# Kernel optimization log

Measured on AMD Instinct MI355X. Metric: run time of the kernel, lower is better.

Reference implementation:

```python
import jax, jax.numpy as jnp
import numpy as np

D_MODEL = 1024
N_HEADS = 16
HEAD_DIM = D_MODEL // N_HEADS
Q_PROJ = D_MODEL // 2
KV_PROJ = D_MODEL
INIT_SCALE = 0.02
EPS = 1e-5


def _ln(x, g, b):
    mu = jnp.mean(x, axis=-1, keepdims=True)
    var = jnp.mean(jnp.square(x - mu), axis=-1, keepdims=True)
    return (x - mu) * jax.lax.rsqrt(var + EPS) * g + b


def setup_inputs() -> dict:
    key = jax.random.key(0)
    ks = jax.random.split(key, 8)
    B, S = 2, 2048
    x = jax.random.normal(ks[0], (B, S, D_MODEL), dtype=jnp.float32)
    W_dq = INIT_SCALE * jax.random.normal(ks[1], (D_MODEL, Q_PROJ), dtype=jnp.float32)
    W_uq = INIT_SCALE * jax.random.normal(ks[2], (Q_PROJ, D_MODEL), dtype=jnp.float32)
    W_dkv = INIT_SCALE * jax.random.normal(ks[3], (D_MODEL, KV_PROJ), dtype=jnp.float32)
    W_ukv = INIT_SCALE * jax.random.normal(ks[4], (KV_PROJ, 2 * D_MODEL), dtype=jnp.float32)
    wo = INIT_SCALE * jax.random.normal(ks[5], (D_MODEL, D_MODEL), dtype=jnp.float32)
    return {
        "x": x,
        "W_dq": W_dq, "W_uq": W_uq,
        "q_ln_g": jnp.ones((Q_PROJ,), jnp.float32), "q_ln_b": jnp.zeros((Q_PROJ,), jnp.float32),
        "W_dkv": W_dkv, "W_ukv": W_ukv,
        "kv_ln_g": jnp.ones((KV_PROJ,), jnp.float32), "kv_ln_b": jnp.zeros((KV_PROJ,), jnp.float32),
        "preq_g": jnp.ones((D_MODEL,), jnp.float32), "preq_b": jnp.zeros((D_MODEL,), jnp.float32),
        "prekv_g": jnp.ones((D_MODEL,), jnp.float32), "prekv_b": jnp.zeros((D_MODEL,), jnp.float32),
        "wo": wo,
    }


def reference(x, W_dq, W_uq, q_ln_g, q_ln_b, W_dkv, W_ukv, kv_ln_g, kv_ln_b,
              preq_g, preq_b, prekv_g, prekv_b, wo):
    B, S, D = x.shape
    H, dh = N_HEADS, HEAD_DIM
    # Q path: pre-norm -> low-rank down -> LN -> up
    x_q = _ln(x, preq_g, preq_b)
    cq = _ln(x_q @ W_dq, q_ln_g, q_ln_b)            # [B,S,D/2]
    Q = (cq @ W_uq).reshape(B, S, H, dh)             # [B,S,H,dh]
    Q = Q / jnp.sqrt(jnp.asarray(dh, x.dtype))
    # KV path: pre-norm -> compress -> LN -> up, split into K,V
    x_kv = _ln(x, prekv_g, prekv_b)
    ckv = _ln(x_kv @ W_dkv, kv_ln_g, kv_ln_b)        # [B,S,D]
    KV = ckv @ W_ukv                                 # [B,S,2D]
    K, V = jnp.split(KV, 2, axis=-1)
    K = K.reshape(B, S, H, dh)
    V = V.reshape(B, S, H, dh)
    # causal attention (scores materialized as in original)
    scores = jnp.einsum('bqhd,bkhd->bhqk', Q, K)     # [B,H,S,S]
    causal = jnp.tril(jnp.ones((S, S), dtype=bool))  # True where allowed
    scores = jnp.where(causal[None, None], scores, jnp.asarray(-jnp.inf, scores.dtype))
    attn = jax.nn.softmax(scores, axis=-1)
    out = jnp.einsum('bhqk,bkhd->bqhd', attn, V).reshape(B, S, D)
    return out @ wo.T
```

## Files before the change

kernel.cpp:

```cpp
#include <hip/hip_runtime.h>
#include <hip/hip_bf16.h>

#define SEQ   2048
#define BATCH 2
#define NROWS 4096
#define DM    1024
#define NHEAD 16
#define DH    64
#define QP    512
#define KVP   1024
#define CH    8

typedef unsigned short us;
using bf16x8 = __attribute__((ext_vector_type(8))) __bf16;
using f32x4  = __attribute__((ext_vector_type(4))) float;

__device__ __forceinline__ us f2bf(float f) {
  union { __hip_bfloat16 h; us u; } cv;
  cv.h = __float2bfloat16(f);
  return cv.u;
}
__device__ __forceinline__ float bf2f(us u) {
  union { unsigned int u32; float f; } cv;
  cv.u32 = ((unsigned int)u) << 16;
  return cv.f;
}
__device__ __forceinline__ float loadp(const void* p, long i, int isbf) {
  return isbf ? bf2f(((const us*)p)[i]) : ((const float*)p)[i];
}
__device__ __forceinline__ void async16(const void* g, void* l) {
  __builtin_amdgcn_global_load_lds((__attribute__((address_space(1))) void*)g,
                                   (__attribute__((address_space(3))) void*)l,
                                   16, 0, 0);
}

__global__ void detect_dtype(const us* __restrict__ xu, int* __restrict__ flag) {
  __shared__ int red[256];
  const int tid = threadIdx.x;
  int cnt = 0;
  for (int i = tid; i < 4096; i += 256) {
    const int e = (xu[i] >> 7) & 0xff;
    if (e == 0 || (e >= 100 && e <= 134)) cnt++;
  }
  red[tid] = cnt;
  __syncthreads();
  for (int s = 128; s; s >>= 1) {
    if (tid < s) red[tid] += red[tid + s];
    __syncthreads();
  }
  if (tid == 0) *flag = (red[0] >= 3900) ? 1 : 0;
}

struct TD { const void* in; us* out; int R, C, nt, trans; };

__global__ __launch_bounds__(256) void prep_weights(TD t0, TD t1, TD t2, TD t3, TD t4,
                                                    const int* __restrict__ flag) {
  __shared__ us tile[32][33];
  int lin = blockIdx.x;
  TD t = t0;
  if (lin >= t.nt) { lin -= t.nt; t = t1;
    if (lin >= t.nt) { lin -= t.nt; t = t2;
      if (lin >= t.nt) { lin -= t.nt; t = t3;
        if (lin >= t.nt) { lin -= t.nt; t = t4; } } } }
  const int isbf = *flag;
  const int ntx = t.C >> 5;
  const int by = lin / ntx, bx = lin - by * ntx;
  const int tx = threadIdx.x & 31, ty = threadIdx.x >> 5;
  const long r0 = (long)by * 32, c0 = (long)bx * 32;
  if (t.trans) {
#pragma unroll
    for (int i = 0; i < 32; i += 8)
      tile[ty + i][tx] = isbf ? ((const us*)t.in)[(r0 + ty + i) * t.C + c0 + tx]
                              : f2bf(((const float*)t.in)[(r0 + ty + i) * t.C + c0 + tx]);
    __syncthreads();
#pragma unroll
    for (int i = 0; i < 32; i += 8)
      t.out[(c0 + ty + i) * t.R + r0 + tx] = tile[tx][ty + i];
  } else {
#pragma unroll
    for (int i = 0; i < 32; i += 8)
      t.out[(r0 + ty + i) * t.C + c0 + tx] =
          isbf ? ((const us*)t.in)[(r0 + ty + i) * t.C + c0 + tx]
               : f2bf(((const float*)t.in)[(r0 + ty + i) * t.C + c0 + tx]);
  }
}

__global__ void zero_f32(float4* __restrict__ p, int n4) {
  int i = blockIdx.x * blockDim.x + threadIdx.x;
  const int stride = gridDim.x * blockDim.x;
  const float4 z = {0.f, 0.f, 0.f, 0.f};
  for (; i < n4; i += stride) p[i] = z;
}

__global__ __launch_bounds__(256) void ln_dual(
    const void* __restrict__ xin,
    const void* __restrict__ g1, const void* __restrict__ b1,
    const void* __restrict__ g2, const void* __restrict__ b2,
    us* __restrict__ out1, us* __restrict__ out2,
    const int* __restrict__ flag)
{
  const long row = blockIdx.x;
  const int tid = threadIdx.x;
  const int isbf = *flag;
  float v[4];
  float s = 0.f, s2 = 0.f;
#pragma unroll
  for (int i = 0; i < 4; i++) {
    const long c = tid + i * 256;
    const float t = loadp(xin, row * 1024 + c, isbf);
    v[i] = t; s += t; s2 += t * t;
  }
#pragma unroll
  for (int off = 32; off > 0; off >>= 1) {
    s  += __shfl_down(s,  off);
    s2 += __shfl_down(s2, off);
  }
  __shared__ float red[8];
  __shared__ float musd[2];
  const int wave = tid >> 6, lane = tid & 63;
  if (lane == 0) { red[wave] = s; red[4 + wave] = s2; }
  __syncthreads();
  if (tid == 0) {
    const float ts = red[0] + red[1] + red[2] + red[3];
    const float t2 = red[4] + red[5] + red[6] + red[7];
    const float mu = ts * (1.f / 1024.f);
    const float var = t2 * (1.f / 1024.f) - mu * mu;
    musd[0] = mu; musd[1] = rsqrtf(var + 1e-5f);
  }
  __syncthreads();
  const float mu = musd[0], rs = musd[1];
#pragma unroll
  for (int i = 0; i < 4; i++) {
    const long c = tid + i * 256;
    const float nrm = (v[i] - mu) * rs;
    out1[row * 1024 + c] = f2bf(nrm * loadp(g1, c, isbf) + loadp(b1, c, isbf));
    out2[row * 1024 + c] = f2bf(nrm * loadp(g2, c, isbf) + loadp(b2, c, isbf));
  }
}

template<int C>
__device__ __forceinline__ void ln_body(const us* __restrict__ in,
                                        const void* __restrict__ g, const void* __restrict__ b,
                                        us* __restrict__ out, long row, int tid, int isbf) {
  constexpr int NP = C / 256;
  float v[NP];
  float s = 0.f, s2 = 0.f;
#pragma unroll
  for (int i = 0; i < NP; i++) {
    const float t = bf2f(in[row * C + tid + i * 256]);
    v[i] = t; s += t; s2 += t * t;
  }
#pragma unroll
  for (int off = 32; off > 0; off >>= 1) {
    s  += __shfl_down(s,  off);
    s2 += __shfl_down(s2, off);
  }
  __shared__ float red[8];
  __shared__ float musd[2];
  const int wave = tid >> 6, lane = tid & 63;
  if (lane == 0) { red[wave] = s; red[4 + wave] = s2; }
  __syncthreads();
  if (tid == 0) {
    const float ts = red[0] + red[1] + red[2] + red[3];
    const float t2 = red[4] + red[5] + red[6] + red[7];
    const float mu = ts * (1.f / C);
    const float var = t2 * (1.f / C) - mu * mu;
    musd[0] = mu; musd[1] = rsqrtf(var + 1e-5f);
  }
  __syncthreads();
  const float mu = musd[0], rs = musd[1];
#pragma unroll
  for (int i = 0; i < NP; i++) {
    const long c = tid + i * 256;
    out[row * C + c] = f2bf((v[i] - mu) * rs * loadp(g, c, isbf) + loadp(b, c, isbf));
  }
}

__global__ __launch_bounds__(256) void ln_rows_pair(
    const us* __restrict__ inq, const void* __restrict__ qg, const void* __restrict__ qb,
    us* __restrict__ outq,
    const us* __restrict__ inkv, const void* __restrict__ kvg, const void* __restrict__ kvb,
    us* __restrict__ outkv,
    const int* __restrict__ flag)
{
  const int isbf = *flag;
  if (blockIdx.x < NROWS)
    ln_body<512>(inq, qg, qb, outq, blockIdx.x, threadIdx.x, isbf);
  else
    ln_body<1024>(inkv, kvg, kvb, outkv, blockIdx.x - NROWS, threadIdx.x, isbf);
}

struct GD { const us* A; const us* Bt; void* C; int N, K, nxs; float scale; int omode; };

__global__ __launch_bounds__(256) void gemm_mt(GD g0, GD g1, int nb0,
                                               const int* __restrict__ flag) {
  __shared__ us As[128 * 32];
  __shared__ us Bs[128 * 32];
  GD g;
  int lin = blockIdx.x;
  if (lin < nb0) g = g0; else { g = g1; lin -= nb0; }
  const int by = lin >> g.nxs;
  const int bx = lin - (by << g.nxs);
  const int N = g.N, K = g.K;

  const int tid  = threadIdx.x;
  const int lane = tid & 63;
  const int wave = tid >> 6;
  const int n16  = lane & 15;
  const int quad = lane >> 4;
  const long m0 = (long)by * 128;
  const long n0 = (long)bx * 128;
  const int wm = (wave >> 1) * 64;
  const int wn = (wave & 1) * 64;

  const f32x4 zero = {0.f, 0.f, 0.f, 0.f};
  f32x4 acc[4][4];
#pragma unroll
  for (int i = 0; i < 4; i++)
#pragma unroll
    for (int j = 0; j < 4; j++) acc[i][j] = zero;

  const int srow = tid >> 2;
  const int scol = (tid & 3) * 8;
  const us* Ag0 = g.A  + (m0 + srow) * K + scol;
  const us* Ag1 = g.A  + (m0 + 64 + srow) * K + scol;
  const us* Bg0 = g.Bt + (n0 + srow) * K + scol;
  const us* Bg1 = g.Bt + (n0 + 64 + srow) * K + scol;
  us* As0 = As + srow * 32 + scol;
  us* As1 = As + (64 + srow) * 32 + scol;
  us* Bs0 = Bs + srow * 32 + scol;
  us* Bs1 = Bs + (64 + srow) * 32 + scol;

  for (int k0 = 0; k0 < K; k0 += 32) {
    async16(Ag0 + k0, As0);
    async16(Ag1 + k0, As1);
    async16(Bg0 + k0, Bs0);
    async16(Bg1 + k0, Bs1);
    __syncthreads();
    bf16x8 af[4], bfv[4];
#pragma unroll
    for (int i = 0; i < 4; i++)
      af[i] = *(const bf16x8*)(As + (wm + i * 16 + n16) * 32 + quad * 8);
#pragma unroll
    for (int j = 0; j < 4; j++)
      bfv[j] = *(const bf16x8*)(Bs + (wn + j * 16 + n16) * 32 + quad * 8);
#pragma unroll
    for (int i = 0; i < 4; i++)
#pragma unroll
      for (int j = 0; j < 4; j++)
        acc[i][j] = __builtin_amdgcn_mfma_f32_16x16x32_bf16(af[i], bfv[j], acc[i][j], 0, 0, 0);
    __syncthreads();
  }

  const bool obf = (g.omode == 1) || (g.omode == 2 && *flag != 0);
  float* Cf = (float*)g.C;
  us* Cb = (us*)g.C;
#pragma unroll
  for (int i = 0; i < 4; i++) {
    const long row = m0 + wm + i * 16 + quad * 4;
#pragma unroll
    for (int j = 0; j < 4; j++) {
      const long col = n0 + wn + j * 16 + n16;
#pragma unroll
      for (int r = 0; r < 4; r++) {
        const float v = acc[i][j][r] * g.scale;
        if (obf) Cb[(row + r) * N + col] = f2bf(v);
        else     Cf[(row + r) * N + col] = v;
      }
    }
  }
}

__global__ __launch_bounds__(256) void flash_attn(
    const us* __restrict__ Q, const us* __restrict__ KV,
    float* __restrict__ Oacc, float* __restrict__ Lacc)
{
  __shared__ us Ks[64 * 72];
  __shared__ us Vt[64 * 72];
  __shared__ us Ps[4][16 * 72];

  int lin = blockIdx.x;
  int qt = 31, nc = 0;
  for (; qt >= 0; --qt) { nc = (qt >> 3) + 1; if (lin < nc) break; lin -= nc; }
  const int chunk = lin;
  const int kt0 = chunk * CH;
  const int kt1 = min(kt0 + CH, qt + 1);

  const int h   = blockIdx.y;
  const int bb  = blockIdx.z;
  const int tid = threadIdx.x;
  const int lane = tid & 63;
  const int wave = tid >> 6;
  const int n16 = lane & 15;
  const int quad = lane >> 4;
  const int qbase = qt * 64;
  const long rowQ0 = (long)bb * SEQ;

  bf16x8 aq[2];
  {
    const long gq = (rowQ0 + qbase + wave * 16 + n16) * DM + h * DH;
    aq[0] = *(const bf16x8*)(Q + gq + quad * 8);
    aq[1] = *(const bf16x8*)(Q + gq + 32 + quad * 8);
  }

  const f32x4 zero = {0.f, 0.f, 0.f, 0.f};
  f32x4 oacc[4];
#pragma unroll
  for (int d = 0; d < 4; d++) oacc[d] = zero;
  float rsum[4] = {0.f, 0.f, 0.f, 0.f};

  const int kk_key = tid >> 3;
  const int kk_d8  = (tid & 7) * 8;
  const int vd  = tid & 63;
  const int vkb = (tid >> 6) * 8;

  const us* kgb = KV + (rowQ0 + kk_key) * 2048 + h * DH + kk_d8;
  const us* vgb = KV + (rowQ0 + vkb) * 2048 + KVP + h * DH + vd;

  uint4 kpre0, kpre1;
  us vraw[16];
  auto loadKV = [&](int kt) {
    const us* kg = kgb + (long)kt * (64 * 2048);
    kpre0 = *(const uint4*)kg;
    kpre1 = *(const uint4*)(kg + 32 * 2048);
    const us* vg = vgb + (long)kt * (64 * 2048);
#pragma unroll
    for (int j = 0; j < 8; j++) vraw[j] = vg[j * 2048];
    const us* vg2 = vg + 32 * 2048;
#pragma unroll
    for (int j = 0; j < 8; j++) vraw[8 + j] = vg2[j * 2048];
  };
  loadKV(kt0);

  for (int kt = kt0; kt < kt1; kt++) {
    __syncthreads();
    *(uint4*)(Ks + kk_key * 72 + kk_d8)        = kpre0;
    *(uint4*)(Ks + (kk_key + 32) * 72 + kk_d8) = kpre1;
    {
      uint4 p0, p1;
      p0.x = (unsigned)vraw[0]  | ((unsigned)vraw[1]  << 16);
      p0.y = (unsigned)vraw[2]  | ((unsigned)vraw[3]  << 16);
      p0.z = (unsigned)vraw[4]  | ((unsigned)vraw[5]  << 16);
      p0.w = (unsigned)vraw[6]  | ((unsigned)vraw[7]  << 16);
      p1.x = (unsigned)vraw[8]  | ((unsigned)vraw[9]  << 16);
      p1.y = (unsigned)vraw[10] | ((unsigned)vraw[11] << 16);
      p1.z = (unsigned)vraw[12] | ((unsigned)vraw[13] << 16);
      p1.w = (unsigned)vraw[14] | ((unsigned)vraw[15] << 16);
      *(uint4*)(Vt + vd * 72 + vkb)      = p0;
      *(uint4*)(Vt + vd * 72 + vkb + 32) = p1;
    }
    __syncthreads();
    if (kt + 1 < kt1) loadKV(kt + 1);

    f32x4 sv[4];
#pragma unroll
    for (int j = 0; j < 4; j++) {
      const bf16x8 bk0 = *(const bf16x8*)(Ks + (j * 16 + n16) * 72 + quad * 8);
      const bf16x8 bk1 = *(const bf16x8*)(Ks + (j * 16 + n16) * 72 + 32 + quad * 8);
      f32x4 s = zero;
      s = __builtin_amdgcn_mfma_f32_16x16x32_bf16(aq[0], bk0, s, 0, 0, 0);
      s = __builtin_amdgcn_mfma_f32_16x16x32_bf16(aq[1], bk1, s, 0, 0, 0);
      sv[j] = s;
    }

    const int qrow = qbase + wave * 16 + quad * 4;
    if (kt == qt) {
#pragma unroll
      for (int j = 0; j < 4; j++) {
        const int col = qt * 64 + j * 16 + n16;
#pragma unroll
        for (int r = 0; r < 4; r++)
          sv[j][r] = (col <= qrow + r) ? sv[j][r] : -1e30f;
      }
    }

    us* Pw = Ps[wave];
#pragma unroll
    for (int j = 0; j < 4; j++)
#pragma unroll
      for (int r = 0; r < 4; r++) {
        const float p = __builtin_amdgcn_exp2f(sv[j][r]);
        rsum[r] += p;
        Pw[(quad * 4 + r) * 72 + j * 16 + n16] = f2bf(p);
      }
    __asm__ volatile("s_waitcnt lgkmcnt(0)" ::: "memory");

#pragma unroll
    for (int kc = 0; kc < 2; kc++) {
      const bf16x8 ap = *(const bf16x8*)(Pw + n16 * 72 + kc * 32 + quad * 8);
#pragma unroll
      for (int d = 0; d < 4; d++) {
        const bf16x8 bv = *(const bf16x8*)(Vt + (d * 16 + n16) * 72 + kc * 32 + quad * 8);
        oacc[d] = __builtin_amdgcn_mfma_f32_16x16x32_bf16(ap, bv, oacc[d], 0, 0, 0);
      }
    }
  }

#pragma unroll
  for (int off = 1; off < 16; off <<= 1)
#pragma unroll
    for (int r = 0; r < 4; r++)
      rsum[r] += __shfl_xor(rsum[r], off);

  const long row0 = rowQ0 + qbase + wave * 16 + quad * 4;
  if (n16 == 0) {
#pragma unroll
    for (int r = 0; r < 4; r++)
      atomicAdd(&Lacc[(row0 + r) * NHEAD + h], rsum[r]);
  }
#pragma unroll
  for (int r = 0; r < 4; r++) {
    float* dst = Oacc + (row0 + r) * DM + h * DH + n16;
#pragma unroll
    for (int d = 0; d < 4; d++)
      atomicAdd(dst + d * 16, oacc[d][r]);
  }
}

__global__ __launch_bounds__(256) void flash_combine(
    const float* __restrict__ Oacc, const float* __restrict__ Lacc,
    us* __restrict__ O)
{
  __shared__ float invl[NHEAD];
  const long row = blockIdx.x;
  const int tid = threadIdx.x;
  if (tid < NHEAD) invl[tid] = 1.f / Lacc[row * NHEAD + tid];
  __syncthreads();
#pragma unroll
  for (int i = 0; i < 4; i++) {
    const int col = tid + i * 256;
    O[row * DM + col] = f2bf(Oacc[row * DM + col] * invl[col >> 6]);
  }
}

extern "C" void kernel_launch(void* const* d_in, const int* in_sizes, int n_in,
                              void* d_out, int out_size, void* d_ws, size_t ws_size,
                              hipStream_t stream) {
  const void* x      = d_in[0];
  const void* Wdq    = d_in[1];
  const void* Wuq    = d_in[2];
  const void* qg     = d_in[3];
  const void* qb     = d_in[4];
  const void* Wdkv   = d_in[5];
  const void* Wukv   = d_in[6];
  const void* kvg    = d_in[7];
  const void* kvb    = d_in[8];
  const void* preqg  = d_in[9];
  const void* preqb  = d_in[10];
  const void* prekvg = d_in[11];
  const void* prekvb = d_in[12];
  const void* wo     = d_in[13];

  char* ws = (char*)d_ws;
  const long MB = 1 << 20;
  int* flag   = (int*)ws;
  us* wdq_t   = (us*)(ws + 1 * MB);
  us* wuq_t   = (us*)(ws + 2 * MB);
  us* wdkv_t  = (us*)(ws + 3 * MB);
  us* wukv_t  = (us*)(ws + 5 * MB);
  us* wo_c    = (us*)(ws + 9 * MB);
  us* xq      = (us*)(ws + 11 * MB);
  us* xkv     = (us*)(ws + 19 * MB);
  us* tq_bf   = (us*)(ws + 27 * MB);
  us* tkv_bf  = (us*)(ws + 31 * MB);
  float* Oacc = (float*)(ws + 27 * MB);
  float* Lacc = (float*)(ws + 43 * MB);
  us* obuf    = (us*)(ws + 44 * MB);
  us* cq      = (us*)(ws + 52 * MB);
  us* qbuf    = (us*)(ws + 56 * MB);
  us* ckv     = (us*)(ws + 64 * MB);
  us* kv      = (us*)(ws + 72 * MB);

  Lacc = (float*)(ws + 43 * MB);
  obuf = (us*)(ws + 43 * MB + 256 * 1024);
  cq   = (us*)(ws + 43 * MB + 256 * 1024 + 8 * MB);
  qbuf = (us*)(ws + 43 * MB + 256 * 1024 + 12 * MB);
  ckv  = (us*)(ws + 43 * MB + 256 * 1024 + 20 * MB);
  kv   = (us*)(ws + 43 * MB + 256 * 1024 + 28 * MB);

  detect_dtype<<<1, 256, 0, stream>>>((const us*)x, flag);

  {
    TD t0 = { Wdq,  wdq_t,  1024,  512,  512, 1 };
    TD t1 = { Wuq,  wuq_t,   512, 1024,  512, 1 };
    TD t2 = { Wdkv, wdkv_t, 1024, 1024, 1024, 1 };
    TD t3 = { Wukv, wukv_t, 1024, 2048, 2048, 1 };
    TD t4 = { wo,   wo_c,   1024, 1024, 1024, 0 };
    prep_weights<<<5120, 256, 0, stream>>>(t0, t1, t2, t3, t4, flag);
  }

  ln_dual<<<NROWS, 256, 0, stream>>>(x, preqg, preqb, prekvg, prekvb, xq, xkv, flag);

  {
    GD g0 = { xq,  wdq_t,  tq_bf,   512, 1024, 2, 1.f, 1 };
    GD g1 = { xkv, wdkv_t, tkv_bf, 1024, 1024, 3, 1.f, 1 };
    gemm_mt<<<384, 256, 0, stream>>>(g0, g1, 128, flag);
  }

  ln_rows_pair<<<2 * NROWS, 256, 0, stream>>>(tq_bf, qg, qb, cq, tkv_bf, kvg, kvb, ckv, flag);

  zero_f32<<<2048, 256, 0, stream>>>((float4*)Oacc, (16 * 1024 * 1024 + 256 * 1024) / 16);

  {
    GD g0 = { cq,  wuq_t,  qbuf, 1024,  512, 3, 0.125f * 1.44269504f, 1 };
    GD g1 = { ckv, wukv_t, kv,   2048, 1024, 4, 1.f, 1 };
    gemm_mt<<<768, 256, 0, stream>>>(g0, g1, 256, flag);
  }

  flash_attn<<<dim3(80, NHEAD, BATCH), 256, 0, stream>>>(qbuf, kv, Oacc, Lacc);
  flash_combine<<<NROWS, 256, 0, stream>>>(Oacc, Lacc, obuf);

  {
    GD g0 = { obuf, wo_c, d_out, 1024, 1024, 3, 1.f, 2 };
    gemm_mt<<<256, 256, 0, stream>>>(g0, g0, 256, flag);
  }
}
```

Baseline: 296.3 us.

## Fuse weight prep, zeroing and pre-LN into one kernel; unroll GEMM K by two

Merges the weight transpose/convert, the accumulator zeroing and the dual pre-LayerNorm into a single launch that dispatches work by block index, removing two kernel launches. The GEMM now loads two 32-wide K slabs per barrier pair, halving the number of synchronizations at the cost of twice the LDS. The attention kernel swaps the MFMA operand order so each lane holds one query row, which allows packed 4-element P stores and a cheaper row-sum reduction with fewer atomics. Workspace buffers are aliased to reduce the memory footprint, which adds a risk of overlap hazards between stages.

```diff
diff --git a/kernel.cpp b/kernel.cpp
--- a/kernel.cpp
+++ b/kernel.cpp
@@ -12,6 +12,7 @@
 #define CH    8
 
 typedef unsigned short us;
+typedef ushort4 us4;
 using bf16x8 = __attribute__((ext_vector_type(8))) __bf16;
 using f32x4  = __attribute__((ext_vector_type(4))) float;
 
@@ -53,55 +54,56 @@
 
 struct TD { const void* in; us* out; int R, C, nt, trans; };
 
-__global__ __launch_bounds__(256) void prep_weights(TD t0, TD t1, TD t2, TD t3, TD t4,
-                                                    const int* __restrict__ flag) {
-  __shared__ us tile[32][33];
-  int lin = blockIdx.x;
-  TD t = t0;
-  if (lin >= t.nt) { lin -= t.nt; t = t1;
-    if (lin >= t.nt) { lin -= t.nt; t = t2;
-      if (lin >= t.nt) { lin -= t.nt; t = t3;
-        if (lin >= t.nt) { lin -= t.nt; t = t4; } } } }
-  const int isbf = *flag;
-  const int ntx = t.C >> 5;
-  const int by = lin / ntx, bx = lin - by * ntx;
-  const int tx = threadIdx.x & 31, ty = threadIdx.x >> 5;
-  const long r0 = (long)by * 32, c0 = (long)bx * 32;
-  if (t.trans) {
-#pragma unroll
-    for (int i = 0; i < 32; i += 8)
-      tile[ty + i][tx] = isbf ? ((const us*)t.in)[(r0 + ty + i) * t.C + c0 + tx]
-                              : f2bf(((const float*)t.in)[(r0 + ty + i) * t.C + c0 + tx]);
-    __syncthreads();
-#pragma unroll
-    for (int i = 0; i < 32; i += 8)
-      t.out[(c0 + ty + i) * t.R + r0 + tx] = tile[tx][ty + i];
-  } else {
-#pragma unroll
-    for (int i = 0; i < 32; i += 8)
-      t.out[(r0 + ty + i) * t.C + c0 + tx] =
-          isbf ? ((const us*)t.in)[(r0 + ty + i) * t.C + c0 + tx]
-               : f2bf(((const float*)t.in)[(r0 + ty + i) * t.C + c0 + tx]);
-  }
-}
-
-__global__ void zero_f32(float4* __restrict__ p, int n4) {
-  int i = blockIdx.x * blockDim.x + threadIdx.x;
-  const int stride = gridDim.x * blockDim.x;
-  const float4 z = {0.f, 0.f, 0.f, 0.f};
-  for (; i < n4; i += stride) p[i] = z;
-}
-
-__global__ __launch_bounds__(256) void ln_dual(
+__global__ __launch_bounds__(256) void stage0(
+    TD t0, TD t1, TD t2, TD t3, TD t4,
+    float4* __restrict__ zp, int n4,
     const void* __restrict__ xin,
     const void* __restrict__ g1, const void* __restrict__ b1,
     const void* __restrict__ g2, const void* __restrict__ b2,
     us* __restrict__ out1, us* __restrict__ out2,
     const int* __restrict__ flag)
 {
-  const long row = blockIdx.x;
+  __shared__ us tile[32][33];
+  __shared__ float red[8];
+  __shared__ float musd[2];
   const int tid = threadIdx.x;
   const int isbf = *flag;
+  int lin = blockIdx.x;
+
+  if (lin < 5120) {
+    TD t = t0;
+    if (lin >= t.nt) { lin -= t.nt; t = t1;
+      if (lin >= t.nt) { lin -= t.nt; t = t2;
+        if (lin >= t.nt) { lin -= t.nt; t = t3;
+          if (lin >= t.nt) { lin -= t.nt; t = t4; } } } }
+    const int ntx = t.C >> 5;
+    const int by = lin / ntx, bx = lin - by * ntx;
+    const int tx = tid & 31, ty = tid >> 5;
+    const long r0 = (long)by * 32, c0 = (long)bx * 32;
+    if (t.trans) {
+#pragma unroll
+      for (int i = 0; i < 32; i += 8)
+        tile[ty + i][tx] = isbf ? ((const us*)t.in)[(r0 + ty + i) * t.C + c0 + tx]
+                                : f2bf(((const float*)t.in)[(r0 + ty + i) * t.C + c0 + tx]);
+      __syncthreads();
+#pragma unroll
+      for (int i = 0; i < 32; i += 8)
+        t.out[(c0 + ty + i) * t.R + r0 + tx] = tile[tx][ty + i];
+    } else {
+#pragma unroll
+      for (int i = 0; i < 32; i += 8)
+        t.out[(r0 + ty + i) * t.C + c0 + tx] =
+            isbf ? ((const us*)t.in)[(r0 + ty + i) * t.C + c0 + tx]
+                 : f2bf(((const float*)t.in)[(r0 + ty + i) * t.C + c0 + tx]);
+    }
+    return;
+  }
+  if (lin < 6144) {
+    const float4 z = {0.f, 0.f, 0.f, 0.f};
+    for (int i = (lin - 5120) * 256 + tid; i < n4; i += 1024 * 256) zp[i] = z;
+    return;
+  }
+  const long row = lin - 6144;
   float v[4];
   float s = 0.f, s2 = 0.f;
 #pragma unroll
@@ -115,8 +117,6 @@
     s  += __shfl_down(s,  off);
     s2 += __shfl_down(s2, off);
   }
-  __shared__ float red[8];
-  __shared__ float musd[2];
   const int wave = tid >> 6, lane = tid & 63;
   if (lane == 0) { red[wave] = s; red[4 + wave] = s2; }
   __syncthreads();
@@ -194,8 +194,8 @@
 
 __global__ __launch_bounds__(256) void gemm_mt(GD g0, GD g1, int nb0,
                                                const int* __restrict__ flag) {
-  __shared__ us As[128 * 32];
-  __shared__ us Bs[128 * 32];
+  __shared__ us As[2][128 * 32];
+  __shared__ us Bs[2][128 * 32];
   GD g;
   int lin = blockIdx.x;
   if (lin < nb0) g = g0; else { g = g1; lin -= nb0; }
@@ -226,29 +226,33 @@
   const us* Ag1 = g.A  + (m0 + 64 + srow) * K + scol;
   const us* Bg0 = g.Bt + (n0 + srow) * K + scol;
   const us* Bg1 = g.Bt + (n0 + 64 + srow) * K + scol;
-  us* As0 = As + srow * 32 + scol;
-  us* As1 = As + (64 + srow) * 32 + scol;
-  us* Bs0 = Bs + srow * 32 + scol;
-  us* Bs1 = Bs + (64 + srow) * 32 + scol;
-
-  for (int k0 = 0; k0 < K; k0 += 32) {
-    async16(Ag0 + k0, As0);
-    async16(Ag1 + k0, As1);
-    async16(Bg0 + k0, Bs0);
-    async16(Bg1 + k0, Bs1);
+  const int lds_off = srow * 32 + scol;
+
+  for (int k0 = 0; k0 < K; k0 += 64) {
+#pragma unroll
+    for (int s = 0; s < 2; s++) {
+      const int ks = k0 + s * 32;
+      async16(Ag0 + ks, As[s] + lds_off);
+      async16(Ag1 + ks, As[s] + 2048 + lds_off);
+      async16(Bg0 + ks, Bs[s] + lds_off);
+      async16(Bg1 + ks, Bs[s] + 2048 + lds_off);
+    }
     __syncthreads();
-    bf16x8 af[4], bfv[4];
-#pragma unroll
-    for (int i = 0; i < 4; i++)
-      af[i] = *(const bf16x8*)(As + (wm + i * 16 + n16) * 32 + quad * 8);
-#pragma unroll
-    for (int j = 0; j < 4; j++)
-      bfv[j] = *(const bf16x8*)(Bs + (wn + j * 16 + n16) * 32 + quad * 8);
-#pragma unroll
-    for (int i = 0; i < 4; i++)
+#pragma unroll
+    for (int s = 0; s < 2; s++) {
+      bf16x8 af[4], bfv[4];
+#pragma unroll
+      for (int i = 0; i < 4; i++)
+        af[i] = *(const bf16x8*)(As[s] + (wm + i * 16 + n16) * 32 + quad * 8);
 #pragma unroll
       for (int j = 0; j < 4; j++)
-        acc[i][j] = __builtin_amdgcn_mfma_f32_16x16x32_bf16(af[i], bfv[j], acc[i][j], 0, 0, 0);
+        bfv[j] = *(const bf16x8*)(Bs[s] + (wn + j * 16 + n16) * 32 + quad * 8);
+#pragma unroll
+      for (int i = 0; i < 4; i++)
+#pragma unroll
+        for (int j = 0; j < 4; j++)
+          acc[i][j] = __builtin_amdgcn_mfma_f32_16x16x32_bf16(af[i], bfv[j], acc[i][j], 0, 0, 0);
+    }
     __syncthreads();
   }
 
@@ -307,7 +311,7 @@
   f32x4 oacc[4];
 #pragma unroll
   for (int d = 0; d < 4; d++) oacc[d] = zero;
-  float rsum[4] = {0.f, 0.f, 0.f, 0.f};
+  float rsum = 0.f;
 
   const int kk_key = tid >> 3;
   const int kk_d8  = (tid & 7) * 8;
@@ -355,34 +359,37 @@
     f32x4 sv[4];
 #pragma unroll
     for (int j = 0; j < 4; j++) {
-      const bf16x8 bk0 = *(const bf16x8*)(Ks + (j * 16 + n16) * 72 + quad * 8);
-      const bf16x8 bk1 = *(const bf16x8*)(Ks + (j * 16 + n16) * 72 + 32 + quad * 8);
+      const bf16x8 ak0 = *(const bf16x8*)(Ks + (j * 16 + n16) * 72 + quad * 8);
+      const bf16x8 ak1 = *(const bf16x8*)(Ks + (j * 16 + n16) * 72 + 32 + quad * 8);
       f32x4 s = zero;
-      s = __builtin_amdgcn_mfma_f32_16x16x32_bf16(aq[0], bk0, s, 0, 0, 0);
-      s = __builtin_amdgcn_mfma_f32_16x16x32_bf16(aq[1], bk1, s, 0, 0, 0);
+      s = __builtin_amdgcn_mfma_f32_16x16x32_bf16(ak0, aq[0], s, 0, 0, 0);
+      s = __builtin_amdgcn_mfma_f32_16x16x32_bf16(ak1, aq[1], s, 0, 0, 0);
       sv[j] = s;
     }
 
-    const int qrow = qbase + wave * 16 + quad * 4;
     if (kt == qt) {
+      const int qrl = wave * 16 + n16;
 #pragma unroll
       for (int j = 0; j < 4; j++) {
-        const int col = qt * 64 + j * 16 + n16;
+        const int kl = j * 16 + quad * 4;
 #pragma unroll
         for (int r = 0; r < 4; r++)
-          sv[j][r] = (col <= qrow + r) ? sv[j][r] : -1e30f;
+          sv[j][r] = (kl + r <= qrl) ? sv[j][r] : -1e30f;
       }
     }
 
     us* Pw = Ps[wave];
 #pragma unroll
-    for (int j = 0; j < 4; j++)
-#pragma unroll
-      for (int r = 0; r < 4; r++) {
-        const float p = __builtin_amdgcn_exp2f(sv[j][r]);
-        rsum[r] += p;
-        Pw[(quad * 4 + r) * 72 + j * 16 + n16] = f2bf(p);
-      }
+    for (int j = 0; j < 4; j++) {
+      const float p0 = __builtin_amdgcn_exp2f(sv[j][0]);
+      const float p1 = __builtin_amdgcn_exp2f(sv[j][1]);
+      const float p2 = __builtin_amdgcn_exp2f(sv[j][2]);
+      const float p3 = __builtin_amdgcn_exp2f(sv[j][3]);
+      rsum += (p0 + p1) + (p2 + p3);
+      us4 pk;
+      pk.x = f2bf(p0); pk.y = f2bf(p1); pk.z = f2bf(p2); pk.w = f2bf(p3);
+      *(us4*)(Pw + n16 * 72 + j * 16 + quad * 4) = pk;
+    }
     __asm__ volatile("s_waitcnt lgkmcnt(0)" ::: "memory");
 
 #pragma unroll
@@ -396,21 +403,15 @@
     }
   }
 
-#pragma unroll
-  for (int off = 1; off < 16; off <<= 1)
-#pragma unroll
-    for (int r = 0; r < 4; r++)
-      rsum[r] += __shfl_xor(rsum[r], off);
-
-  const long row0 = rowQ0 + qbase + wave * 16 + quad * 4;
-  if (n16 == 0) {
-#pragma unroll
-    for (int r = 0; r < 4; r++)
-      atomicAdd(&Lacc[(row0 + r) * NHEAD + h], rsum[r]);
-  }
+  rsum += __shfl_xor(rsum, 16);
+  rsum += __shfl_xor(rsum, 32);
+
+  const long rw0 = rowQ0 + qbase + wave * 16;
+  if (quad == 0)
+    atomicAdd(&Lacc[(rw0 + n16) * NHEAD + h], rsum);
 #pragma unroll
   for (int r = 0; r < 4; r++) {
-    float* dst = Oacc + (row0 + r) * DM + h * DH + n16;
+    float* dst = Oacc + (rw0 + quad * 4 + r) * DM + h * DH + n16;
 #pragma unroll
     for (int d = 0; d < 4; d++)
       atomicAdd(dst + d * 16, oacc[d][r]);
@@ -461,22 +462,15 @@
   us* wo_c    = (us*)(ws + 9 * MB);
   us* xq      = (us*)(ws + 11 * MB);
   us* xkv     = (us*)(ws + 19 * MB);
-  us* tq_bf   = (us*)(ws + 27 * MB);
-  us* tkv_bf  = (us*)(ws + 31 * MB);
   float* Oacc = (float*)(ws + 27 * MB);
   float* Lacc = (float*)(ws + 43 * MB);
-  us* obuf    = (us*)(ws + 44 * MB);
-  us* cq      = (us*)(ws + 52 * MB);
-  us* qbuf    = (us*)(ws + 56 * MB);
-  us* ckv     = (us*)(ws + 64 * MB);
-  us* kv      = (us*)(ws + 72 * MB);
-
-  Lacc = (float*)(ws + 43 * MB);
-  obuf = (us*)(ws + 43 * MB + 256 * 1024);
-  cq   = (us*)(ws + 43 * MB + 256 * 1024 + 8 * MB);
-  qbuf = (us*)(ws + 43 * MB + 256 * 1024 + 12 * MB);
-  ckv  = (us*)(ws + 43 * MB + 256 * 1024 + 20 * MB);
-  kv   = (us*)(ws + 43 * MB + 256 * 1024 + 28 * MB);
+  us* obuf    = (us*)(ws + 43 * MB + 256 * 1024);
+  us* tq_bf   = obuf;
+  us* cq      = (us*)(ws + 43 * MB + 256 * 1024 + 8 * MB);
+  us* qbuf    = (us*)(ws + 43 * MB + 256 * 1024 + 12 * MB);
+  us* tkv_bf  = qbuf;
+  us* ckv     = (us*)(ws + 43 * MB + 256 * 1024 + 20 * MB);
+  us* kv      = (us*)(ws + 43 * MB + 256 * 1024 + 28 * MB);
 
   detect_dtype<<<1, 256, 0, stream>>>((const us*)x, flag);
 
@@ -486,10 +480,11 @@
     TD t2 = { Wdkv, wdkv_t, 1024, 1024, 1024, 1 };
     TD t3 = { Wukv, wukv_t, 1024, 2048, 2048, 1 };
     TD t4 = { wo,   wo_c,   1024, 1024, 1024, 0 };
-    prep_weights<<<5120, 256, 0, stream>>>(t0, t1, t2, t3, t4, flag);
-  }
-
-  ln_dual<<<NROWS, 256, 0, stream>>>(x, preqg, preqb, prekvg, prekvb, xq, xkv, flag);
+    const int n4 = (16 * 1024 * 1024 + 256 * 1024) / 16;
+    stage0<<<10240, 256, 0, stream>>>(t0, t1, t2, t3, t4,
+                                      (float4*)Oacc, n4,
+                                      x, preqg, preqb, prekvg, prekvb, xq, xkv, flag);
+  }
 
   {
     GD g0 = { xq,  wdq_t,  tq_bf,   512, 1024, 2, 1.f, 1 };
@@ -499,8 +494,6 @@
 
   ln_rows_pair<<<2 * NROWS, 256, 0, stream>>>(tq_bf, qg, qb, cq, tkv_bf, kvg, kvb, ckv, flag);
 
-  zero_f32<<<2048, 256, 0, stream>>>((float4*)Oacc, (16 * 1024 * 1024 + 256 * 1024) / 16);
-
   {
     GD g0 = { cq,  wuq_t,  qbuf, 1024,  512, 3, 0.125f * 1.44269504f, 1 };
     GD g1 = { ckv, wukv_t, kv,   2048, 1024, 4, 1.f, 1 };
```

After: 274.3 us. 7.4% less time.
